# Kernel tuning notes

Hardware: AMD Instinct MI355X
Metric: run time of the kernel (lower is better)

Reference implementation:

```python
import jax, jax.numpy as jnp
import numpy as np

N = 50000      # nodes
E = 1600000    # edges (before self loops)
F_IN = 1433    # input features (Cora)
H1, C1 = 8, 8  # layer1: heads, out channels per head
C2 = 7         # layer2: classes (heads=1, concat=False)
SLOPE = 0.2    # PyG GATConv default negative_slope


def _gat_layer(x, src, dst, W, a_src, a_dst, b, heads, out_ch, concat):
    """PyG-style GATConv (eval mode, self loops already in src/dst)."""
    n = x.shape[0]
    h = (x @ W).reshape(n, heads, out_ch)                 # [N,H,C]
    alpha_s = jnp.einsum('nhc,hc->nh', h, a_src)          # [N,H]
    alpha_d = jnp.einsum('nhc,hc->nh', h, a_dst)          # [N,H]
    e = jax.nn.leaky_relu(alpha_s[src] + alpha_d[dst], SLOPE)  # [E,H]
    # segment softmax over incoming edges per destination node
    m = jax.ops.segment_max(e, dst, num_segments=n)       # [N,H]
    ex = jnp.exp(e - m[dst])
    denom = jax.ops.segment_sum(ex, dst, num_segments=n)  # [N,H]
    alpha = ex / (denom[dst] + 1e-16)                     # [E,H]
    out = jax.ops.segment_sum(h[src] * alpha[..., None], dst, num_segments=n)  # [N,H,C]
    out = out.reshape(n, heads * out_ch) if concat else out.mean(axis=1)
    return out + b


def setup_inputs() -> dict:
    key = jax.random.key(0)
    ks = jax.random.split(key, 10)
    x = jax.random.normal(ks[0], (N, F_IN), jnp.float32)
    edge_index = jax.random.randint(ks[1], (2, E), 0, N, jnp.int32)
    s = 0.1
    return {
        'x': x,
        'edge_index': edge_index,
        'W1': jax.random.normal(ks[2], (F_IN, H1 * C1), jnp.float32) * s,
        'att_src1': jax.random.normal(ks[3], (H1, C1), jnp.float32) * s,
        'att_dst1': jax.random.normal(ks[4], (H1, C1), jnp.float32) * s,
        'b1': jnp.zeros((H1 * C1,), jnp.float32),
        'W2': jax.random.normal(ks[5], (H1 * C1, C2), jnp.float32) * s,
        'att_src2': jax.random.normal(ks[6], (1, C2), jnp.float32) * s,
        'att_dst2': jax.random.normal(ks[7], (1, C2), jnp.float32) * s,
        'b2': jnp.zeros((C2,), jnp.float32),
    }


def reference(x, edge_index, W1, att_src1, att_dst1, b1, W2, att_src2, att_dst2, b2):
    loop = jnp.arange(N, dtype=edge_index.dtype)
    src = jnp.concatenate([edge_index[0], loop])   # add_self_loops=True
    dst = jnp.concatenate([edge_index[1], loop])
    h = _gat_layer(x, src, dst, W1, att_src1, att_dst1, b1, H1, C1, True)   # [N,64]
    h = jax.nn.elu(h)
    out = _gat_layer(h, src, dst, W2, att_src2, att_dst2, b2, 1, C2, False)  # [N,7]
    return jax.nn.log_softmax(out, axis=1)
```

## Files before the change

### kernel.cpp

```cpp
#include <hip/hip_runtime.h>
#include <hip/hip_bf16.h>

static constexpr int NN      = 50000;
static constexpr int FIN     = 1433;
static constexpr int KPAD    = 1440;
static constexpr int NB_SCAN = (NN + 255) / 256;
static constexpr int L1B     = NN / 4;

typedef __bf16 bf16x8 __attribute__((ext_vector_type(8)));
typedef float  f32x4  __attribute__((ext_vector_type(4)));

__device__ __forceinline__ float leaky02(float v){ return v >= 0.f ? v : 0.2f * v; }
__device__ __forceinline__ float bflo(unsigned u){ return __uint_as_float(u << 16); }
__device__ __forceinline__ float bfhi(unsigned u){ return __uint_as_float(u & 0xffff0000u); }

__device__ __forceinline__ void gld_lds4(const float* g, float* l){
    __builtin_amdgcn_global_load_lds(
        (const __attribute__((address_space(1))) unsigned int*)g,
        (__attribute__((address_space(3))) unsigned int*)l, 4, 0, 0);
}

__global__ __launch_bounds__(256) void k_prep(const float* __restrict__ W1,
                                              __bf16* __restrict__ w1h, __bf16* __restrict__ w1l,
                                              int* __restrict__ deg){
    int bid = blockIdx.x;
    if (bid < 64){
        int c = bid;
        for (int k = threadIdx.x; k < KPAD; k += 256){
            float v = (k < FIN) ? W1[(size_t)k * 64 + c] : 0.f;
            __bf16 hi = (__bf16)v;
            w1h[(size_t)c * KPAD + k] = hi;
            w1l[(size_t)c * KPAD + k] = (__bf16)(v - (float)hi);
        }
    } else {
        int i = (bid - 64) * 256 + threadIdx.x;
        if (i < NN) deg[i] = 0;
    }
}

__global__ __launch_bounds__(256) void k_rank(const int* __restrict__ dst, int* __restrict__ deg,
                                              int* __restrict__ rank, int E){
    int base = blockIdx.x * 1024 + threadIdx.x;
    int d[4]; bool v[4];
    #pragma unroll
    for (int i = 0; i < 4; ++i){
        int e = base + i * 256;
        v[i] = e < E;
        d[i] = v[i] ? dst[e] : 0;
    }
    int r[4];
    #pragma unroll
    for (int i = 0; i < 4; ++i)
        if (v[i]) r[i] = atomicAdd(&deg[d[i]], 1);
    #pragma unroll
    for (int i = 0; i < 4; ++i)
        if (v[i]) rank[base + i * 256] = r[i];
}

__global__ __launch_bounds__(256) void k_scan1(const int* __restrict__ deg, int* __restrict__ bsum){
    __shared__ int red[256];
    int i = blockIdx.x * 256 + threadIdx.x;
    red[threadIdx.x] = (i < NN) ? deg[i] : 0;
    __syncthreads();
    for (int off = 128; off > 0; off >>= 1){
        if (threadIdx.x < off) red[threadIdx.x] += red[threadIdx.x + off];
        __syncthreads();
    }
    if (threadIdx.x == 0) bsum[blockIdx.x] = red[0];
}

__global__ __launch_bounds__(256) void k_scan3(const int* __restrict__ deg, const int* __restrict__ bsum,
                                               int* __restrict__ row_off){
    __shared__ int s[256];
    int t = threadIdx.x;
    int i = blockIdx.x * 256 + t;
    s[t] = (t < blockIdx.x) ? bsum[t] : 0;
    __syncthreads();
    for (int off = 128; off > 0; off >>= 1){
        if (t < off) s[t] += s[t + off];
        __syncthreads();
    }
    int bofs = s[0];
    __syncthreads();
    int d = (i < NN) ? deg[i] : 0;
    s[t] = d;
    __syncthreads();
    for (int off = 1; off < 256; off <<= 1){
        int v = s[t];
        int a = (t >= off) ? s[t - off] : 0;
        __syncthreads();
        s[t] = v + a;
        __syncthreads();
    }
    int excl = s[t] - d + bofs;
    if (i < NN){
        row_off[i] = excl;
        if (i == NN - 1) row_off[NN] = excl + d;
    }
}

__global__ __launch_bounds__(256) void k_scatter(const int* __restrict__ src, const int* __restrict__ dst,
                                                 const int* __restrict__ rank, const int* __restrict__ row_off,
                                                 int* __restrict__ csr, int E){
    int base = blockIdx.x * 1024 + threadIdx.x;
    int d[4], r[4], sv[4]; bool v[4];
    #pragma unroll
    for (int i = 0; i < 4; ++i){
        int e = base + i * 256;
        v[i] = e < E;
        if (v[i]){ d[i] = dst[e]; r[i] = rank[e]; sv[i] = src[e]; }
    }
    int ro[4];
    #pragma unroll
    for (int i = 0; i < 4; ++i)
        if (v[i]) ro[i] = row_off[d[i]];
    #pragma unroll
    for (int i = 0; i < 4; ++i)
        if (v[i]) csr[ro[i] + r[i]] = sv[i];
}

__global__ __launch_bounds__(256, 4) void k_gemm1(const float* __restrict__ x,
    const __bf16* __restrict__ w1h, const __bf16* __restrict__ w1l,
    __bf16* __restrict__ Hb)
{
    __shared__ float  As[64 * 68];
    __shared__ __bf16 AH[64 * 72];
    __shared__ __bf16 AL[64 * 72];
    const int tid  = threadIdx.x;
    const int w    = tid >> 6;
    const int lane = tid & 63;
    const int lr   = lane & 15;
    const int lk   = lane >> 4;
    const int rbase = blockIdx.x * 64;
    const int cr = tid >> 2;
    const int cg = (tid & 3) * 16;

    unsigned rowoff[16];
    #pragma unroll
    for (int i = 0; i < 16; ++i){
        int rg = rbase + w * 16 + i; if (rg >= NN) rg = NN - 1;
        rowoff[i] = (unsigned)rg * (unsigned)FIN + (unsigned)lane;
    }

    const __bf16* bh_p = w1h + (size_t)(w * 16 + lr) * KPAD + lk * 8;
    const __bf16* bl_p = w1l + (size_t)(w * 16 + lr) * KPAD + lk * 8;

    f32x4 acc[4] = {{0,0,0,0},{0,0,0,0},{0,0,0,0},{0,0,0,0}};

    #pragma unroll
    for (int i = 0; i < 16; ++i)
        gld_lds4(x + rowoff[i], &As[(w * 16 + i) * 68]);
    __syncthreads();

    for (int kb = 0; kb < 22; ++kb){
        {
            const float* rp = &As[cr * 68 + cg];
            f32x4 v[4];
            #pragma unroll
            for (int j = 0; j < 4; ++j) v[j] = *(const f32x4*)(rp + j * 4);
            bf16x8 hv0, hv1, lv0, lv1;
            #pragma unroll
            for (int j = 0; j < 2; ++j){
                #pragma unroll
                for (int e = 0; e < 4; ++e){
                    float a0 = v[2 * j][e], a1 = v[2 * j + 1][e];
                    __bf16 h0 = (__bf16)a0, h1 = (__bf16)a1;
                    if (j == 0){ hv0[e] = h0; hv0[e + 4] = h1;
                                 lv0[e] = (__bf16)(a0 - (float)h0);
                                 lv0[e + 4] = (__bf16)(a1 - (float)h1); }
                    else       { hv1[e] = h0; hv1[e + 4] = h1;
                                 lv1[e] = (__bf16)(a0 - (float)h0);
                                 lv1[e + 4] = (__bf16)(a1 - (float)h1); }
                }
            }
            *(bf16x8*)&AH[cr * 72 + cg]     = hv0;
            *(bf16x8*)&AH[cr * 72 + cg + 8] = hv1;
            *(bf16x8*)&AL[cr * 72 + cg]     = lv0;
            *(bf16x8*)&AL[cr * 72 + cg + 8] = lv1;
        }
        __syncthreads();

        if (kb < 21){
            const float* gsrc = x + (kb + 1) * 64;
            #pragma unroll
            for (int i = 0; i < 16; ++i)
                gld_lds4(gsrc + rowoff[i], &As[(w * 16 + i) * 68]);
        }

        const int kA = kb * 64;
        bf16x8 bh0 = *(const bf16x8*)(bh_p + kA);
        bf16x8 bl0 = *(const bf16x8*)(bl_p + kA);
        bf16x8 bh1 = *(const bf16x8*)(bh_p + kA + 32);
        bf16x8 bl1 = *(const bf16x8*)(bl_p + kA + 32);
        #pragma unroll
        for (int ks = 0; ks < 2; ++ks){
            bf16x8 bh = ks ? bh1 : bh0;
            bf16x8 bl = ks ? bl1 : bl0;
            #pragma unroll
            for (int t = 0; t < 4; ++t){
                const int ao = (t * 16 + lr) * 72 + ks * 32 + lk * 8;
                bf16x8 ah = *(const bf16x8*)&AH[ao];
                bf16x8 al = *(const bf16x8*)&AL[ao];
                acc[t] = __builtin_amdgcn_mfma_f32_16x16x32_bf16(ah, bh, acc[t], 0, 0, 0);
                acc[t] = __builtin_amdgcn_mfma_f32_16x16x32_bf16(al, bh, acc[t], 0, 0, 0);
                acc[t] = __builtin_amdgcn_mfma_f32_16x16x32_bf16(ah, bl, acc[t], 0, 0, 0);
            }
        }
        __syncthreads();
    }

    {
        bf16x8 bh = *(const bf16x8*)(bh_p + 1408);
        bf16x8 bl = *(const bf16x8*)(bl_p + 1408);
        #pragma unroll
        for (int t = 0; t < 4; ++t){
            int rg = rbase + t * 16 + lr; if (rg >= NN) rg = NN - 1;
            const float* xr = x + (size_t)rg * FIN;
            bf16x8 ah, al;
            #pragma unroll
            for (int e = 0; e < 8; ++e){
                int k = 1408 + lk * 8 + e;
                float v = (k < FIN) ? xr[k] : 0.f;
                __bf16 h = (__bf16)v;
                ah[e] = h; al[e] = (__bf16)(v - (float)h);
            }
            acc[t] = __builtin_amdgcn_mfma_f32_16x16x32_bf16(ah, bh, acc[t], 0, 0, 0);
            acc[t] = __builtin_amdgcn_mfma_f32_16x16x32_bf16(al, bh, acc[t], 0, 0, 0);
            acc[t] = __builtin_amdgcn_mfma_f32_16x16x32_bf16(ah, bl, acc[t], 0, 0, 0);
        }
    }

    const int col = w * 16 + lr;
    #pragma unroll
    for (int t = 0; t < 4; ++t){
        #pragma unroll
        for (int r = 0; r < 4; ++r){
            int row = rbase + t * 16 + lk * 4 + r;
            if (row < NN) Hb[(size_t)row * 64 + col] = (__bf16)acc[t][r];
        }
    }
}

__global__ __launch_bounds__(256, 8) void k_layer1(const float* __restrict__ a_s,
    const float* __restrict__ a_d,
    const __bf16* __restrict__ Hb, const int* __restrict__ row_off, const int* __restrict__ csr,
    const float* __restrict__ b1, __bf16* __restrict__ x2b)
{
    const int d  = blockIdx.x * 4 + (threadIdx.x >> 6);
    const int l  = threadIdx.x & 63;
    const int e8 = l >> 3;
    const int c8 = l & 7;
    const int c0 = c8 * 8;

    float asw[8], adw[8];
    #pragma unroll
    for (int j = 0; j < 8; ++j){ asw[j] = a_s[c0 + j]; adw[j] = a_d[c0 + j]; }

    float den = 0.f;
    float a[8] = {0.f,0.f,0.f,0.f,0.f,0.f,0.f,0.f};
    float adv;
    {
        uint4 hs = *(const uint4*)&Hb[(size_t)d * 64 + c0];
        float hv[8] = { bflo(hs.x), bfhi(hs.x), bflo(hs.y), bfhi(hs.y),
                        bflo(hs.z), bfhi(hs.z), bflo(hs.w), bfhi(hs.w) };
        float ad_ = 0.f, as_ = 0.f;
        #pragma unroll
        for (int j = 0; j < 8; ++j){
            ad_ = fmaf(hv[j], adw[j], ad_);
            as_ = fmaf(hv[j], asw[j], as_);
        }
        adv = ad_;
        if (e8 == 0){
            float p0 = __expf(leaky02(as_ + adv) - 20.f);
            den = p0;
            #pragma unroll
            for (int j = 0; j < 8; ++j) a[j] = p0 * hv[j];
        }
    }

    const int beg = row_off[d], end = row_off[d + 1];
    const int nb = (end - beg + 7) >> 3;
    int csrv = 0;
    if (nb > 0){
        int idx = beg + c8; if (idx >= end) idx = end - 1;
        csrv = __builtin_nontemporal_load(csr + idx);
    }
    for (int b = 0; b < nb; ++b){
        const int base = beg + b * 8;
        int ncsr = 0;
        if (b + 1 < nb){
            int idx = base + 8 + c8; if (idx >= end) idx = end - 1;
            ncsr = __builtin_nontemporal_load(csr + idx);
        }
        int s = __shfl(csrv, e8, 8);
        const bool val = (base + e8) < end;
        uint4 hw = make_uint4(0u,0u,0u,0u);
        if (val) hw = *(const uint4*)&Hb[(size_t)s * 64 + c0];
        if (val){
            float g[8] = { bflo(hw.x), bfhi(hw.x), bflo(hw.y), bfhi(hw.y),
                           bflo(hw.z), bfhi(hw.z), bflo(hw.w), bfhi(hw.w) };
            float av = 0.f;
            #pragma unroll
            for (int j = 0; j < 8; ++j) av = fmaf(g[j], asw[j], av);
            float p = __expf(leaky02(av + adv) - 20.f);
            den += p;
            #pragma unroll
            for (int j = 0; j < 8; ++j) a[j] = fmaf(p, g[j], a[j]);
        }
        csrv = ncsr;
    }

    #pragma unroll
    for (int m = 8; m <= 32; m <<= 1){
        den += __shfl_xor(den, m, 64);
        #pragma unroll
        for (int j = 0; j < 8; ++j) a[j] += __shfl_xor(a[j], m, 64);
    }

    if (e8 == 0){
        float inv = 1.f / den;
        __bf16 ov[8];
        #pragma unroll
        for (int j = 0; j < 8; ++j){
            float v = a[j] * inv + b1[c0 + j];
            ov[j] = (__bf16)((v > 0.f) ? v : (__expf(v) - 1.f));
        }
        *(uint4*)&x2b[(size_t)d * 64 + c0] = *(uint4*)ov;
    }
}

__global__ __launch_bounds__(256) void k_gemm2(const __bf16* __restrict__ x2b, const float* __restrict__ W2,
    const float* __restrict__ aw_in, const float* __restrict__ dw_in,
    __bf16* __restrict__ h2b, float* __restrict__ ad2)
{
    __shared__ float w2s[448];
    __shared__ float aw[7], dw[7];
    int tid = threadIdx.x;
    for (int i = tid; i < 448; i += 256) w2s[i] = W2[i];
    if (tid < 7){ aw[tid] = aw_in[tid]; dw[tid] = dw_in[tid]; }
    __syncthreads();
    int n = blockIdx.x * 256 + tid;
    if (n >= NN) return;
    const uint4* xp = (const uint4*)(x2b + (size_t)n * 64);
    float acc[7] = {0.f,0.f,0.f,0.f,0.f,0.f,0.f};
    #pragma unroll
    for (int q = 0; q < 8; ++q){
        uint4 v = xp[q];
        float vv[8] = { bflo(v.x), bfhi(v.x), bflo(v.y), bfhi(v.y),
                        bflo(v.z), bfhi(v.z), bflo(v.w), bfhi(v.w) };
        #pragma unroll
        for (int u = 0; u < 8; ++u){
            int k = q * 8 + u;
            #pragma unroll
            for (int c = 0; c < 7; ++c) acc[c] = fmaf(vv[u], w2s[k * 7 + c], acc[c]);
        }
    }
    float s = 0.f, d = 0.f;
    #pragma unroll
    for (int c = 0; c < 7; ++c){ s = fmaf(acc[c], aw[c], s); d = fmaf(acc[c], dw[c], d); }
    __bf16 rec[8];
    #pragma unroll
    for (int c = 0; c < 7; ++c) rec[c] = (__bf16)acc[c];
    rec[7] = (__bf16)s;
    *(uint4*)&h2b[(size_t)n * 8] = *(uint4*)rec;
    ad2[n] = d;
}

__global__ __launch_bounds__(256, 8) void k_layer2(const float* __restrict__ ad2,
    const __bf16* __restrict__ h2b, const int* __restrict__ row_off, const int* __restrict__ csr,
    const float* __restrict__ b2, float* __restrict__ out)
{
    int tid  = threadIdx.x;
    int node = blockIdx.x * 32 + (tid >> 3);
    int sl   = tid & 7;
    if (node >= NN) return;
    float adv = ad2[node];

    float den = 0.f;
    float a[7] = {0.f,0.f,0.f,0.f,0.f,0.f,0.f};
    {
        uint4 hs = *(const uint4*)&h2b[(size_t)node * 8];
        float h[8] = { bflo(hs.x), bfhi(hs.x), bflo(hs.y), bfhi(hs.y),
                       bflo(hs.z), bfhi(hs.z), bflo(hs.w), bfhi(hs.w) };
        if (sl == 0){
            float p0 = __expf(leaky02(h[7] + adv) - 20.f);
            den = p0;
            #pragma unroll
            for (int c = 0; c < 7; ++c) a[c] = p0 * h[c];
        }
    }

    const int beg = row_off[node], end = row_off[node + 1];
    const int nb = (end - beg + 7) >> 3;
    int csrv = 0;
    if (nb > 0){
        int idx = beg + sl; if (idx >= end) idx = end - 1;
        csrv = __builtin_nontemporal_load(csr + idx);
    }
    for (int b = 0; b < nb; ++b){
        const int base = beg + b * 8;
        int ncsr = 0;
        if (b + 1 < nb){
            int idx = base + 8 + sl; if (idx >= end) idx = end - 1;
            ncsr = __builtin_nontemporal_load(csr + idx);
        }
        const bool val = (base + sl) < end;
        uint4 hw = make_uint4(0u,0u,0u,0u);
        if (val) hw = *(const uint4*)&h2b[(size_t)csrv * 8];
        if (val){
            float g[8] = { bflo(hw.x), bfhi(hw.x), bflo(hw.y), bfhi(hw.y),
                           bflo(hw.z), bfhi(hw.z), bflo(hw.w), bfhi(hw.w) };
            float p = __expf(leaky02(g[7] + adv) - 20.f);
            den += p;
            #pragma unroll
            for (int c = 0; c < 7; ++c) a[c] = fmaf(p, g[c], a[c]);
        }
        csrv = ncsr;
    }

    #pragma unroll
    for (int m = 1; m <= 4; m <<= 1){
        den += __shfl_xor(den, m, 64);
        #pragma unroll
        for (int c = 0; c < 7; ++c) a[c] += __shfl_xor(a[c], m, 64);
    }

    if (sl == 0){
        float inv = 1.f / den;
        float v[7];
        #pragma unroll
        for (int c = 0; c < 7; ++c) v[c] = a[c] * inv + b2[c];
        float mx = v[0];
        #pragma unroll
        for (int c = 1; c < 7; ++c) mx = fmaxf(mx, v[c]);
        float s7 = 0.f;
        #pragma unroll
        for (int c = 0; c < 7; ++c) s7 += __expf(v[c] - mx);
        float lg = mx + __logf(s7);
        float* op = &out[(size_t)node * 7];
        #pragma unroll
        for (int c = 0; c < 7; ++c) op[c] = v[c] - lg;
    }
}

extern "C" void kernel_launch(void* const* d_in, const int* in_sizes, int n_in,
                              void* d_out, int out_size, void* d_ws, size_t ws_size,
                              hipStream_t stream)
{
    (void)n_in; (void)out_size; (void)ws_size;
    const float* x      = (const float*)d_in[0];
    const int*   ei     = (const int*)d_in[1];
    const int    E      = in_sizes[1] / 2;
    const float* W1     = (const float*)d_in[2];
    const float* asrc1  = (const float*)d_in[3];
    const float* adst1  = (const float*)d_in[4];
    const float* b1     = (const float*)d_in[5];
    const float* W2     = (const float*)d_in[6];
    const float* asrc2  = (const float*)d_in[7];
    const float* adst2  = (const float*)d_in[8];
    const float* b2     = (const float*)d_in[9];
    float* out = (float*)d_out;

    char* p = (char*)d_ws;
    auto alloc = [&](size_t bytes) -> void* {
        void* r = (void*)p;
        p += (bytes + 255) & ~(size_t)255;
        return r;
    };
    int*    deg     = (int*)alloc((size_t)NN * 4);
    int*    row_off = (int*)alloc((size_t)(NN + 1) * 4);
    int*    rank    = (int*)alloc((size_t)E * 4);
    int*    bsum    = (int*)alloc((size_t)NB_SCAN * 4);
    int*    csr     = (int*)alloc((size_t)E * 4);
    __bf16* w1h     = (__bf16*)alloc((size_t)64 * KPAD * 2);
    __bf16* w1l     = (__bf16*)alloc((size_t)64 * KPAD * 2);
    __bf16* Hb      = (__bf16*)alloc((size_t)NN * 64 * 2);
    __bf16* x2b     = (__bf16*)alloc((size_t)NN * 64 * 2);
    __bf16* h2b     = (__bf16*)alloc((size_t)NN * 8 * 2);
    float*  ad2     = (float*)alloc((size_t)NN * 4);

    const int* src = ei;
    const int* dst = ei + E;

    k_prep   <<<64 + NB_SCAN, 256, 0, stream>>>(W1, w1h, w1l, deg);
    k_rank   <<<(E + 1023) / 1024, 256, 0, stream>>>(dst, deg, rank, E);
    k_scan1  <<<NB_SCAN, 256, 0, stream>>>(deg, bsum);
    k_scan3  <<<NB_SCAN, 256, 0, stream>>>(deg, bsum, row_off);
    k_scatter<<<(E + 1023) / 1024, 256, 0, stream>>>(src, dst, rank, row_off, csr, E);
    k_gemm1  <<<(NN + 63) / 64, 256, 0, stream>>>(x, w1h, w1l, Hb);
    k_layer1 <<<L1B, 256, 0, stream>>>(asrc1, adst1, Hb, row_off, csr, b1, x2b);
    k_gemm2  <<<(NN + 255) / 256, 256, 0, stream>>>(x2b, W2, asrc2, adst2, h2b, ad2);
    k_layer2 <<<(NN + 31) / 32, 256, 0, stream>>>(ad2, h2b, row_off, csr, b2, out);
}
```

Before: 288.8 us.

## Fuse CSR construction into one cooperative kernel with grid syncs

Replaces the five CSR-building kernels (prep, rank, scan1, scan3, scatter) with a single cooperative kernel that uses grid-wide syncs between phases, removing the launch gaps between them. The per-edge rank array is dropped. Scatter now claims slots with atomic cursors after the scan, which changes the order of neighbours within a row. The cost is grid.sync overhead, a fixed 1024-block grid that must fit co-resident, and a second pass of atomics over all edges.

After: 898.0 us. +211.0%, slower.

```diff
diff --git a/kernel.cpp b/kernel.cpp
--- a/kernel.cpp
+++ b/kernel.cpp
@@ -1,11 +1,14 @@
 #include <hip/hip_runtime.h>
 #include <hip/hip_bf16.h>
+#include <hip/hip_cooperative_groups.h>
+namespace cg = cooperative_groups;
 
 static constexpr int NN      = 50000;
 static constexpr int FIN     = 1433;
 static constexpr int KPAD    = 1440;
 static constexpr int NB_SCAN = (NN + 255) / 256;
 static constexpr int L1B     = NN / 4;
+static constexpr int CSRG    = 1024;
 
 typedef __bf16 bf16x8 __attribute__((ext_vector_type(8)));
 typedef float  f32x4  __attribute__((ext_vector_type(4)));
@@ -20,103 +23,87 @@
         (__attribute__((address_space(3))) unsigned int*)l, 4, 0, 0);
 }
 
-__global__ __launch_bounds__(256) void k_prep(const float* __restrict__ W1,
-                                              __bf16* __restrict__ w1h, __bf16* __restrict__ w1l,
-                                              int* __restrict__ deg){
-    int bid = blockIdx.x;
-    if (bid < 64){
-        int c = bid;
-        for (int k = threadIdx.x; k < KPAD; k += 256){
-            float v = (k < FIN) ? W1[(size_t)k * 64 + c] : 0.f;
-            __bf16 hi = (__bf16)v;
-            w1h[(size_t)c * KPAD + k] = hi;
-            w1l[(size_t)c * KPAD + k] = (__bf16)(v - (float)hi);
-        }
-    } else {
-        int i = (bid - 64) * 256 + threadIdx.x;
-        if (i < NN) deg[i] = 0;
-    }
-}
-
-__global__ __launch_bounds__(256) void k_rank(const int* __restrict__ dst, int* __restrict__ deg,
-                                              int* __restrict__ rank, int E){
-    int base = blockIdx.x * 1024 + threadIdx.x;
-    int d[4]; bool v[4];
-    #pragma unroll
-    for (int i = 0; i < 4; ++i){
-        int e = base + i * 256;
-        v[i] = e < E;
-        d[i] = v[i] ? dst[e] : 0;
-    }
-    int r[4];
-    #pragma unroll
-    for (int i = 0; i < 4; ++i)
-        if (v[i]) r[i] = atomicAdd(&deg[d[i]], 1);
-    #pragma unroll
-    for (int i = 0; i < 4; ++i)
-        if (v[i]) rank[base + i * 256] = r[i];
-}
-
-__global__ __launch_bounds__(256) void k_scan1(const int* __restrict__ deg, int* __restrict__ bsum){
-    __shared__ int red[256];
-    int i = blockIdx.x * 256 + threadIdx.x;
-    red[threadIdx.x] = (i < NN) ? deg[i] : 0;
-    __syncthreads();
-    for (int off = 128; off > 0; off >>= 1){
-        if (threadIdx.x < off) red[threadIdx.x] += red[threadIdx.x + off];
-        __syncthreads();
-    }
-    if (threadIdx.x == 0) bsum[blockIdx.x] = red[0];
-}
-
-__global__ __launch_bounds__(256) void k_scan3(const int* __restrict__ deg, const int* __restrict__ bsum,
-                                               int* __restrict__ row_off){
+__global__ __launch_bounds__(256) void k_csr(const float* __restrict__ W1,
+    __bf16* __restrict__ w1h, __bf16* __restrict__ w1l,
+    const int* __restrict__ src, const int* __restrict__ dst,
+    int* __restrict__ deg, int* __restrict__ bsum,
+    int* __restrict__ row_off, int* __restrict__ cursor,
+    int* __restrict__ csr, int E)
+{
+    cg::grid_group grid = cg::this_grid();
+    const int gsize = gridDim.x * 256;
+    const int gtid  = blockIdx.x * 256 + threadIdx.x;
     __shared__ int s[256];
-    int t = threadIdx.x;
-    int i = blockIdx.x * 256 + t;
-    s[t] = (t < blockIdx.x) ? bsum[t] : 0;
-    __syncthreads();
-    for (int off = 128; off > 0; off >>= 1){
-        if (t < off) s[t] += s[t + off];
-        __syncthreads();
-    }
-    int bofs = s[0];
-    __syncthreads();
-    int d = (i < NN) ? deg[i] : 0;
-    s[t] = d;
-    __syncthreads();
-    for (int off = 1; off < 256; off <<= 1){
-        int v = s[t];
-        int a = (t >= off) ? s[t - off] : 0;
-        __syncthreads();
-        s[t] = v + a;
-        __syncthreads();
-    }
-    int excl = s[t] - d + bofs;
-    if (i < NN){
-        row_off[i] = excl;
-        if (i == NN - 1) row_off[NN] = excl + d;
-    }
-}
-
-__global__ __launch_bounds__(256) void k_scatter(const int* __restrict__ src, const int* __restrict__ dst,
-                                                 const int* __restrict__ rank, const int* __restrict__ row_off,
-                                                 int* __restrict__ csr, int E){
-    int base = blockIdx.x * 1024 + threadIdx.x;
-    int d[4], r[4], sv[4]; bool v[4];
-    #pragma unroll
-    for (int i = 0; i < 4; ++i){
-        int e = base + i * 256;
-        v[i] = e < E;
-        if (v[i]){ d[i] = dst[e]; r[i] = rank[e]; sv[i] = src[e]; }
-    }
-    int ro[4];
-    #pragma unroll
-    for (int i = 0; i < 4; ++i)
-        if (v[i]) ro[i] = row_off[d[i]];
-    #pragma unroll
-    for (int i = 0; i < 4; ++i)
-        if (v[i]) csr[ro[i] + r[i]] = sv[i];
+
+    for (int i = gtid; i < NN; i += gsize) deg[i] = 0;
+    for (int i = gtid; i < 64 * KPAD; i += gsize){
+        int c = i / KPAD, k = i - c * KPAD;
+        float v = (k < FIN) ? W1[(size_t)k * 64 + c] : 0.f;
+        __bf16 hi = (__bf16)v;
+        w1h[(size_t)c * KPAD + k] = hi;
+        w1l[(size_t)c * KPAD + k] = (__bf16)(v - (float)hi);
+    }
+    grid.sync();
+
+    for (int i = gtid; i < E; i += gsize) atomicAdd(&deg[dst[i]], 1);
+    grid.sync();
+
+    for (int c = blockIdx.x; c < NB_SCAN; c += gridDim.x){
+        int i = c * 256 + threadIdx.x;
+        s[threadIdx.x] = (i < NN) ? deg[i] : 0;
+        __syncthreads();
+        for (int off = 128; off > 0; off >>= 1){
+            if (threadIdx.x < off) s[threadIdx.x] += s[threadIdx.x + off];
+            __syncthreads();
+        }
+        if (threadIdx.x == 0) bsum[c] = s[0];
+        __syncthreads();
+    }
+    grid.sync();
+
+    if (blockIdx.x == 0){
+        int t = threadIdx.x;
+        int v = (t < NB_SCAN) ? bsum[t] : 0;
+        s[t] = v;
+        __syncthreads();
+        for (int off = 1; off < 256; off <<= 1){
+            int x_ = s[t];
+            int add = (t >= off) ? s[t - off] : 0;
+            __syncthreads();
+            s[t] = x_ + add;
+            __syncthreads();
+        }
+        if (t < NB_SCAN) bsum[t] = s[t] - v;
+    }
+    grid.sync();
+
+    for (int c = blockIdx.x; c < NB_SCAN; c += gridDim.x){
+        int t = threadIdx.x;
+        int i = c * 256 + t;
+        int d = (i < NN) ? deg[i] : 0;
+        s[t] = d;
+        __syncthreads();
+        for (int off = 1; off < 256; off <<= 1){
+            int v = s[t];
+            int add = (t >= off) ? s[t - off] : 0;
+            __syncthreads();
+            s[t] = v + add;
+            __syncthreads();
+        }
+        int excl = s[t] - d + bsum[c];
+        if (i < NN){
+            row_off[i] = excl; cursor[i] = excl;
+            if (i == NN - 1) row_off[NN] = excl + d;
+        }
+        __syncthreads();
+    }
+    grid.sync();
+
+    for (int i = gtid; i < E; i += gsize){
+        int dd = dst[i];
+        int pos = atomicAdd(&cursor[dd], 1);
+        csr[pos] = src[i];
+    }
 }
 
 __global__ __launch_bounds__(256, 4) void k_gemm1(const float* __restrict__ x,
@@ -133,7 +120,7 @@
     const int lk   = lane >> 4;
     const int rbase = blockIdx.x * 64;
     const int cr = tid >> 2;
-    const int cg = (tid & 3) * 16;
+    const int cg_ = (tid & 3) * 16;
 
     unsigned rowoff[16];
     #pragma unroll
@@ -154,7 +141,7 @@
 
     for (int kb = 0; kb < 22; ++kb){
         {
-            const float* rp = &As[cr * 68 + cg];
+            const float* rp = &As[cr * 68 + cg_];
             f32x4 v[4];
             #pragma unroll
             for (int j = 0; j < 4; ++j) v[j] = *(const f32x4*)(rp + j * 4);
@@ -173,10 +160,10 @@
                                  lv1[e + 4] = (__bf16)(a1 - (float)h1); }
                 }
             }
-            *(bf16x8*)&AH[cr * 72 + cg]     = hv0;
-            *(bf16x8*)&AH[cr * 72 + cg + 8] = hv1;
-            *(bf16x8*)&AL[cr * 72 + cg]     = lv0;
-            *(bf16x8*)&AL[cr * 72 + cg + 8] = lv1;
+            *(bf16x8*)&AH[cr * 72 + cg_]     = hv0;
+            *(bf16x8*)&AH[cr * 72 + cg_ + 8] = hv1;
+            *(bf16x8*)&AL[cr * 72 + cg_]     = lv0;
+            *(bf16x8*)&AL[cr * 72 + cg_ + 8] = lv1;
         }
         __syncthreads();
 
@@ -450,7 +437,7 @@
     (void)n_in; (void)out_size; (void)ws_size;
     const float* x      = (const float*)d_in[0];
     const int*   ei     = (const int*)d_in[1];
-    const int    E      = in_sizes[1] / 2;
+    int          E      = in_sizes[1] / 2;
     const float* W1     = (const float*)d_in[2];
     const float* asrc1  = (const float*)d_in[3];
     const float* adst1  = (const float*)d_in[4];
@@ -469,7 +456,7 @@
     };
     int*    deg     = (int*)alloc((size_t)NN * 4);
     int*    row_off = (int*)alloc((size_t)(NN + 1) * 4);
-    int*    rank    = (int*)alloc((size_t)E * 4);
+    int*    cursor  = (int*)alloc((size_t)NN * 4);
     int*    bsum    = (int*)alloc((size_t)NB_SCAN * 4);
     int*    csr     = (int*)alloc((size_t)E * 4);
     __bf16* w1h     = (__bf16*)alloc((size_t)64 * KPAD * 2);
@@ -482,11 +469,13 @@
     const int* src = ei;
     const int* dst = ei + E;
 
-    k_prep   <<<64 + NB_SCAN, 256, 0, stream>>>(W1, w1h, w1l, deg);
-    k_rank   <<<(E + 1023) / 1024, 256, 0, stream>>>(dst, deg, rank, E);
-    k_scan1  <<<NB_SCAN, 256, 0, stream>>>(deg, bsum);
-    k_scan3  <<<NB_SCAN, 256, 0, stream>>>(deg, bsum, row_off);
-    k_scatter<<<(E + 1023) / 1024, 256, 0, stream>>>(src, dst, rank, row_off, csr, E);
+    {
+        void* args[] = { (void*)&W1, (void*)&w1h, (void*)&w1l,
+                         (void*)&src, (void*)&dst, (void*)&deg, (void*)&bsum,
+                         (void*)&row_off, (void*)&cursor, (void*)&csr, (void*)&E };
+        hipLaunchCooperativeKernel((const void*)k_csr, dim3(CSRG), dim3(256),
+                                   args, 0, stream);
+    }
     k_gemm1  <<<(NN + 63) / 64, 256, 0, stream>>>(x, w1h, w1l, Hb);
     k_layer1 <<<L1B, 256, 0, stream>>>(asrc1, adst1, Hb, row_off, csr, b1, x2b);
     k_gemm2  <<<(NN + 255) / 256, 256, 0, stream>>>(x2b, W2, asrc2, adst2, h2b, ad2);
```
